# Kernel tuning notes

Hardware: AMD Instinct MI355X
Metric: run time of the kernel (lower is better)

The kernel has to match this reference:

```python
import jax, jax.numpy as jnp
import numpy as np

B = 16          # number of variable-length sequences
T = 131072      # total tokens (sum of lengths)
E = 2048        # embedding_size
O = 1024        # output_size


def setup_inputs() -> dict:
    key = jax.random.key(0)
    kx, kw, kb = jax.random.split(key, 3)
    # random partition of T into B positive segment lengths
    rs = np.random.RandomState(0)
    cuts = np.sort(rs.choice(np.arange(1, T), size=B - 1, replace=False))
    lengths = np.diff(np.concatenate([[0], cuts, [T]])).astype(np.int64)
    x = jax.random.normal(kx, (T, E), dtype=jnp.float32)
    W = jax.random.normal(kw, (E, O), dtype=jnp.float32) * 0.02  # Linear weight (stored transposed)
    b = jnp.zeros((O,), dtype=jnp.float32)                        # Linear bias
    return {"x": x, "W": W, "b": b, "lengths": jnp.asarray(lengths)}


def reference(x, W, b, lengths):
    # Fused segmented mean over ragged sequences, then linear projection.
    T_ = x.shape[0]
    B_ = lengths.shape[0]
    offsets = jnp.cumsum(lengths)                                   # [B] exclusive-end offsets
    seg_ids = jnp.searchsorted(offsets, jnp.arange(T_), side="right")  # [T] segment id per row
    sums = jax.ops.segment_sum(x, seg_ids, num_segments=B_)        # [B, E]
    means = sums / lengths[:, None].astype(x.dtype)                # per-segment mean
    return means @ W + b                                           # [B, O]
```

## Files before the change

kernel.cpp:

```cpp
#include <hip/hip_runtime.h>


#define E_DIM 2048
#define O_DIM 1024
#define R_CHUNK 128

typedef float v4f __attribute__((ext_vector_type(4)));

__global__ __launch_bounds__(256) void seg_partial(const float* __restrict__ x,
                                                   const int* __restrict__ lengths,
                                                   int Bn,
                                                   float* __restrict__ partial) {
    __shared__ int s_start[65];
    __shared__ int s_cbase[65];
    if (threadIdx.x == 0) {
        int off = 0, cb = 0;
        for (int i = 0; i < Bn; ++i) {
            s_start[i] = off; s_cbase[i] = cb;
            const int l = lengths[i];
            off += l; cb += (l + R_CHUNK - 1) / R_CHUNK;
        }
        s_start[Bn] = off; s_cbase[Bn] = cb;
    }
    __syncthreads();

    const int g = blockIdx.x;
    if (g >= s_cbase[Bn]) return;
    int b = 0;
    while (g >= s_cbase[b + 1]) ++b;
    const int r0 = s_start[b] + (g - s_cbase[b]) * R_CHUNK;
    const int r1 = min(r0 + R_CHUNK, s_start[b + 1]);

    const int tx = threadIdx.x;
    v4f a0 = {0.f, 0.f, 0.f, 0.f};
    v4f a1 = {0.f, 0.f, 0.f, 0.f};
    const v4f* p = (const v4f*)(x + (size_t)r0 * E_DIM + tx * 4);
#pragma unroll 4
    for (int r = r0; r < r1; ++r) {
        v4f v0 = __builtin_nontemporal_load(p);
        v4f v1 = __builtin_nontemporal_load(p + 256);
        a0 += v0;
        a1 += v1;
        p += E_DIM / 4;
    }
    v4f* dst = (v4f*)(partial + (size_t)g * E_DIM + tx * 4);
    dst[0]   = a0;
    dst[256] = a1;
}

__global__ __launch_bounds__(256) void reduce_means(const float* __restrict__ partial,
                                                    const int* __restrict__ lengths,
                                                    int Bn,
                                                    float* __restrict__ means) {
    __shared__ int s_cb, s_nch, s_len;
    if (threadIdx.x == 0) {
        const int b = blockIdx.y;
        int cb = 0;
        for (int i = 0; i < b; ++i) cb += (lengths[i] + R_CHUNK - 1) / R_CHUNK;
        s_cb = cb;
        s_len = lengths[b];
        s_nch = (s_len + R_CHUNK - 1) / R_CHUNK;
    }
    __syncthreads();

    const int col = blockIdx.x * 1024 + threadIdx.x * 4;
    const int nch = s_nch;
    v4f acc = {0.f, 0.f, 0.f, 0.f};
    const v4f* p = (const v4f*)(partial + (size_t)s_cb * E_DIM + col);
#pragma unroll 8
    for (int c = 0; c < nch; ++c) {
        acc += *p;
        p += E_DIM / 4;
    }
    acc *= (1.0f / (float)s_len);
    *(v4f*)(means + (size_t)blockIdx.y * E_DIM + col) = acc;
}

__global__ __launch_bounds__(256) void gemm_out(const float* __restrict__ means,
                                                const float* __restrict__ W,
                                                const float* __restrict__ bias,
                                                float* __restrict__ out) {
    const int b      = blockIdx.y;
    const int olocal = threadIdx.x & 63;
    const int eg     = threadIdx.x >> 6;
    const int o      = blockIdx.x * 64 + olocal;

    __shared__ float m_lds[E_DIM];
    __shared__ float red[4][64];
    const v4f* msrc = (const v4f*)(means + (size_t)b * E_DIM);
    for (int i = threadIdx.x; i < E_DIM / 4; i += 256)
        ((v4f*)m_lds)[i] = msrc[i];
    __syncthreads();

    float acc = 0.f;
    const float* wp = W + (size_t)(eg * 512) * O_DIM + o;
    const float* mp = m_lds + eg * 512;
#pragma unroll 8
    for (int i = 0; i < 512; ++i)
        acc += mp[i] * wp[(size_t)i * O_DIM];

    red[eg][olocal] = acc;
    __syncthreads();
    if (eg == 0) {
        const float r = red[0][olocal] + red[1][olocal] + red[2][olocal]
                      + red[3][olocal] + bias[o];
        out[b * O_DIM + o] = r;
    }
}

extern "C" void kernel_launch(void* const* d_in, const int* in_sizes, int n_in,
                              void* d_out, int out_size, void* d_ws, size_t ws_size,
                              hipStream_t stream) {
    const float* x       = (const float*)d_in[0];
    const float* W       = (const float*)d_in[1];
    const float* bias    = (const float*)d_in[2];
    const int*   lengths = (const int*)d_in[3];

    const int Bn = in_sizes[3];
    const int On = in_sizes[2];
    const int En = in_sizes[1] / On;
    const int Tn = in_sizes[0] / En;
    (void)En; (void)out_size; (void)n_in; (void)ws_size;

    const int maxChunks      = (Tn + R_CHUNK - 1) / R_CHUNK;
    const int maxTotalChunks = maxChunks + Bn;

    float* partial = (float*)d_ws;
    float* means   = partial + (size_t)maxTotalChunks * E_DIM;

    seg_partial<<<maxTotalChunks, 256, 0, stream>>>(x, lengths, Bn, partial);

    dim3 g2(E_DIM / 1024, Bn);
    reduce_means<<<g2, 256, 0, stream>>>(partial, lengths, Bn, means);

    dim3 g3(On / 64, Bn);
    gemm_out<<<g3, 256, 0, stream>>>(means, W, bias, (float*)d_out);
}
```

Baseline: 217.1 us.

## Split chunk reduction across more blocks and fold final mean into GEMM

Halves the row chunk size so the streaming pass launches twice as many blocks, and replaces the shared-memory prologue with a per-thread scan of the lengths. The second stage now splits each segment's chunk list eight ways, giving many more blocks. The GEMM kernel sums those eight partials, applies 1/length itself, and uses 512 threads with four independent accumulators. The aim is more parallelism in the reduction stage and more memory-level parallelism in the GEMV. The cost is twice as many partial rows to write and read back, plus redundant per-thread scans of the lengths array.

Result: faster. 201.3 us, median of 2 (-7.3%).

```diff
diff --git a/kernel.cpp b/kernel.cpp
--- a/kernel.cpp
+++ b/kernel.cpp
@@ -3,33 +3,29 @@
 
 #define E_DIM 2048
 #define O_DIM 1024
-#define R_CHUNK 128
+#define R_CHUNK 64
+#define S_SPLIT 8
 
 typedef float v4f __attribute__((ext_vector_type(4)));
 
-__global__ __launch_bounds__(256) void seg_partial(const float* __restrict__ x,
-                                                   const int* __restrict__ lengths,
-                                                   int Bn,
-                                                   float* __restrict__ partial) {
-    __shared__ int s_start[65];
-    __shared__ int s_cbase[65];
-    if (threadIdx.x == 0) {
-        int off = 0, cb = 0;
-        for (int i = 0; i < Bn; ++i) {
-            s_start[i] = off; s_cbase[i] = cb;
-            const int l = lengths[i];
-            off += l; cb += (l + R_CHUNK - 1) / R_CHUNK;
+__global__ __launch_bounds__(256, 8) void seg_partial(const float* __restrict__ x,
+                                                      const int* __restrict__ lengths,
+                                                      int Bn,
+                                                      float* __restrict__ partial) {
+    const int g = blockIdx.x;
+    int off = 0, cb = 0, r0 = 0, r1 = 0, found = 0;
+    for (int i = 0; i < Bn; ++i) {
+        const int l  = lengths[i];
+        const int nc = (l + R_CHUNK - 1) / R_CHUNK;
+        if (g < cb + nc) {
+            r0 = off + (g - cb) * R_CHUNK;
+            r1 = min(r0 + R_CHUNK, off + l);
+            found = 1;
+            break;
         }
-        s_start[Bn] = off; s_cbase[Bn] = cb;
+        off += l; cb += nc;
     }
-    __syncthreads();
-
-    const int g = blockIdx.x;
-    if (g >= s_cbase[Bn]) return;
-    int b = 0;
-    while (g >= s_cbase[b + 1]) ++b;
-    const int r0 = s_start[b] + (g - s_cbase[b]) * R_CHUNK;
-    const int r1 = min(r0 + R_CHUNK, s_start[b + 1]);
+    if (!found) return;
 
     const int tx = threadIdx.x;
     v4f a0 = {0.f, 0.f, 0.f, 0.f};
@@ -48,63 +44,74 @@
     dst[256] = a1;
 }
 
-__global__ __launch_bounds__(256) void reduce_means(const float* __restrict__ partial,
-                                                    const int* __restrict__ lengths,
-                                                    int Bn,
-                                                    float* __restrict__ means) {
-    __shared__ int s_cb, s_nch, s_len;
-    if (threadIdx.x == 0) {
-        const int b = blockIdx.y;
-        int cb = 0;
-        for (int i = 0; i < b; ++i) cb += (lengths[i] + R_CHUNK - 1) / R_CHUNK;
-        s_cb = cb;
-        s_len = lengths[b];
-        s_nch = (s_len + R_CHUNK - 1) / R_CHUNK;
+__global__ __launch_bounds__(256) void reduce_p2(const float* __restrict__ partial,
+                                                 const int* __restrict__ lengths,
+                                                 int Bn,
+                                                 float* __restrict__ p2) {
+    const int b = blockIdx.y;
+    const int s = blockIdx.z;
+    int cb = 0;
+    for (int i = 0; i < b; ++i) cb += (lengths[i] + R_CHUNK - 1) / R_CHUNK;
+    const int nch = (lengths[b] + R_CHUNK - 1) / R_CHUNK;
+    const int c0 = (nch * s) / S_SPLIT;
+    const int c1 = (nch * (s + 1)) / S_SPLIT;
+
+    const int col = blockIdx.x * 1024 + threadIdx.x * 4;
+    v4f acc = {0.f, 0.f, 0.f, 0.f};
+    const v4f* p = (const v4f*)(partial + (size_t)(cb + c0) * E_DIM + col);
+#pragma unroll 8
+    for (int c = c0; c < c1; ++c) {
+        acc += *p;
+        p += E_DIM / 4;
+    }
+    *(v4f*)(p2 + ((size_t)(b * S_SPLIT + s)) * E_DIM + col) = acc;
+}
+
+__global__ __launch_bounds__(512) void gemm_out(const float* __restrict__ p2,
+                                                const float* __restrict__ W,
+                                                const float* __restrict__ bias,
+                                                const int* __restrict__ lengths,
+                                                float* __restrict__ out) {
+    const int b      = blockIdx.y;
+    const int tx     = threadIdx.x;
+    const int olocal = tx & 63;
+    const int eg     = tx >> 6;
+    const int o      = blockIdx.x * 64 + olocal;
+
+    __shared__ float m_lds[E_DIM];
+    __shared__ float red[S_SPLIT][64];
+
+    {
+        const float inv = 1.0f / (float)lengths[b];
+        const int col = tx * 4;
+        const v4f* ps = (const v4f*)(p2 + (size_t)b * S_SPLIT * E_DIM + col);
+        v4f m = {0.f, 0.f, 0.f, 0.f};
+#pragma unroll
+        for (int s = 0; s < S_SPLIT; ++s)
+            m += ps[s * (E_DIM / 4)];
+        m *= inv;
+        *(v4f*)(m_lds + col) = m;
     }
     __syncthreads();
 
-    const int col = blockIdx.x * 1024 + threadIdx.x * 4;
-    const int nch = s_nch;
-    v4f acc = {0.f, 0.f, 0.f, 0.f};
-    const v4f* p = (const v4f*)(partial + (size_t)s_cb * E_DIM + col);
+    float a0 = 0.f, a1 = 0.f, a2 = 0.f, a3 = 0.f;
+    const float* wp = W + (size_t)(eg * 256) * O_DIM + o;
+    const float* mp = m_lds + eg * 256;
 #pragma unroll 8
-    for (int c = 0; c < nch; ++c) {
-        acc += *p;
-        p += E_DIM / 4;
+    for (int i = 0; i < 256; i += 4) {
+        a0 += mp[i + 0] * wp[(size_t)(i + 0) * O_DIM];
+        a1 += mp[i + 1] * wp[(size_t)(i + 1) * O_DIM];
+        a2 += mp[i + 2] * wp[(size_t)(i + 2) * O_DIM];
+        a3 += mp[i + 3] * wp[(size_t)(i + 3) * O_DIM];
     }
-    acc *= (1.0f / (float)s_len);
-    *(v4f*)(means + (size_t)blockIdx.y * E_DIM + col) = acc;
-}
-
-__global__ __launch_bounds__(256) void gemm_out(const float* __restrict__ means,
-                                                const float* __restrict__ W,
-                                                const float* __restrict__ bias,
-                                                float* __restrict__ out) {
-    const int b      = blockIdx.y;
-    const int olocal = threadIdx.x & 63;
-    const int eg     = threadIdx.x >> 6;
-    const int o      = blockIdx.x * 64 + olocal;
-
-    __shared__ float m_lds[E_DIM];
-    __shared__ float red[4][64];
-    const v4f* msrc = (const v4f*)(means + (size_t)b * E_DIM);
-    for (int i = threadIdx.x; i < E_DIM / 4; i += 256)
-        ((v4f*)m_lds)[i] = msrc[i];
+    red[eg][olocal] = (a0 + a1) + (a2 + a3);
     __syncthreads();
 
-    float acc = 0.f;
-    const float* wp = W + (size_t)(eg * 512) * O_DIM + o;
-    const float* mp = m_lds + eg * 512;
-#pragma unroll 8
-    for (int i = 0; i < 512; ++i)
-        acc += mp[i] * wp[(size_t)i * O_DIM];
-
-    red[eg][olocal] = acc;
-    __syncthreads();
-    if (eg == 0) {
-        const float r = red[0][olocal] + red[1][olocal] + red[2][olocal]
-                      + red[3][olocal] + bias[o];
-        out[b * O_DIM + o] = r;
+    if (tx < 64) {
+        float r = bias[blockIdx.x * 64 + tx];
+#pragma unroll
+        for (int s = 0; s < S_SPLIT; ++s) r += red[s][tx];
+        out[b * O_DIM + blockIdx.x * 64 + tx] = r;
     }
 }
 
@@ -126,13 +133,13 @@
     const int maxTotalChunks = maxChunks + Bn;
 
     float* partial = (float*)d_ws;
-    float* means   = partial + (size_t)maxTotalChunks * E_DIM;
+    float* p2      = partial + (size_t)maxTotalChunks * E_DIM;
 
     seg_partial<<<maxTotalChunks, 256, 0, stream>>>(x, lengths, Bn, partial);
 
-    dim3 g2(E_DIM / 1024, Bn);
-    reduce_means<<<g2, 256, 0, stream>>>(partial, lengths, Bn, means);
+    dim3 g2(E_DIM / 1024, Bn, S_SPLIT);
+    reduce_p2<<<g2, 256, 0, stream>>>(partial, lengths, Bn, p2);
 
     dim3 g3(On / 64, Bn);
-    gemm_out<<<g3, 256, 0, stream>>>(means, W, bias, (float*)d_out);
+    gemm_out<<<g3, 512, 0, stream>>>(p2, W, bias, lengths, (float*)d_out);
 }
```
